# Kernel tuning notes

Measured on AMD Instinct MI355X. Metric: run time of the kernel, lower is better.

The kernel has to match this reference:

```python
import jax, jax.numpy as jnp
import numpy as np

N, E, T, H, O, L = 8192, 262144, 256, 2048, 1024, 128


def setup_inputs() -> dict:
    key = jax.random.key(0)
    ks = jax.random.split(key, 24)
    inp = {}
    inp["eeg_nodes"] = jax.random.normal(ks[0], (N, T), dtype=jnp.float32)
    inp["eeg_idx"] = jax.random.randint(ks[1], (2, E), 0, N, dtype=jnp.int32)
    # PyG models.GIN layer widths: [T->2048], [2048->2048], [2048->2048], [2048->1024]
    dims = [(T, H), (H, H), (H, H), (H, O)]
    k = 2
    for l, (din, dh) in enumerate(dims):
        inp[f"w1_{l}"] = jax.random.normal(ks[k], (din, dh), jnp.float32) / np.float32(np.sqrt(din)); k += 1
        inp[f"b1_{l}"] = jnp.zeros((dh,), jnp.float32)
        inp[f"w2_{l}"] = jax.random.normal(ks[k], (dh, dh), jnp.float32) / np.float32(np.sqrt(dh)); k += 1
        inp[f"b2_{l}"] = jnp.zeros((dh,), jnp.float32)
    inp["wm"] = jax.random.normal(ks[k], (O, L), jnp.float32) / np.float32(np.sqrt(O)); k += 1
    inp["bm"] = jnp.zeros((L,), jnp.float32)
    inp["wv"] = jax.random.normal(ks[k], (O, L), jnp.float32) / np.float32(np.sqrt(O)); k += 1
    inp["bv"] = jnp.zeros((L,), jnp.float32)
    # reparameterize noise (torch.randn_like) made explicit for determinism
    inp["eps"] = jax.random.normal(ks[k + 1], (N, L), jnp.float32)
    return inp


def _gin_conv(x, src, dst, w1, b1, w2, b2):
    # GINConv, eps=0: mlp((1+0)*x + sum_{j->i} x_j); MLP = Linear-ReLU-Linear (no norm)
    agg = jax.ops.segment_sum(x[src], dst, num_segments=x.shape[0])  # [N, d]
    h = jax.nn.relu((x + agg) @ w1 + b1)
    return h @ w2 + b2


def reference(eeg_nodes, eeg_idx, w1_0, b1_0, w2_0, b2_0, w1_1, b1_1, w2_1, b2_1,
              w1_2, b1_2, w2_2, b2_2, w1_3, b1_3, w2_3, b2_3, wm, bm, wv, bv, eps):
    src, dst = eeg_idx[0], eeg_idx[1]
    layers = [(w1_0, b1_0, w2_0, b2_0), (w1_1, b1_1, w2_1, b2_1),
              (w1_2, b1_2, w2_2, b2_2), (w1_3, b1_3, w2_3, b2_3)]
    x = eeg_nodes
    for i, (w1, b1, w2, b2) in enumerate(layers):
        x = _gin_conv(x, src, dst, w1, b1, w2, b2)
        if i < len(layers) - 1:  # BasicGNN: ReLU between convs, not after last
            x = jax.nn.relu(x)
    mean = x @ wm + bm
    var = x @ wv + bv
    z = mean + var * eps  # reparameterize
    return (z, mean, var)
```

## Files before the change

kernel.cpp:

```cpp
#include <hip/hip_runtime.h>

#define NN 8192
#define EE 262144
#define TT 256
#define HH 2048
#define OO 1024
#define LL 128
#define NW 10

typedef __bf16 bf16_t;
typedef __bf16 bf16x8_t __attribute__((ext_vector_type(8)));
typedef float f32x4_t __attribute__((ext_vector_type(4)));

__device__ __forceinline__ void async16(void* lds, const void* g) {
  __builtin_amdgcn_global_load_lds(
      (const __attribute__((address_space(1))) void*)g,
      (__attribute__((address_space(3))) void*)lds, 16, 0, 0);
}


__global__ __launch_bounds__(256) void count_deg_kernel(const int* __restrict__ dst,
                                                        int* __restrict__ deg) {
  int e = blockIdx.x * 256 + threadIdx.x;
  if (e < EE) atomicAdd(&deg[dst[e]], 1);
}

__global__ __launch_bounds__(1024) void scan_kernel(const int* __restrict__ deg,
                                                    int* __restrict__ rs) {
  __shared__ int s[1024];
  int t = threadIdx.x;
  int pre[8];
  int sum = 0;
#pragma unroll
  for (int j = 0; j < 8; ++j) { pre[j] = sum; sum += deg[t * 8 + j]; }
  s[t] = sum;
  __syncthreads();
  for (int off = 1; off < 1024; off <<= 1) {
    int add = (t >= off) ? s[t - off] : 0;
    __syncthreads();
    s[t] += add;
    __syncthreads();
  }
  int base = (t == 0) ? 0 : s[t - 1];
#pragma unroll
  for (int j = 0; j < 8; ++j) rs[t * 8 + j] = base + pre[j];
  if (t == 1023) rs[8192] = s[1023];
}

__global__ __launch_bounds__(256) void fill_csr_kernel(const int* __restrict__ src,
                                                       const int* __restrict__ dst,
                                                       const int* __restrict__ rs,
                                                       int* __restrict__ cur,
                                                       int* __restrict__ csr) {
  int e = blockIdx.x * 256 + threadIdx.x;
  if (e >= EE) return;
  int d = dst[e];
  int p = atomicAdd(&cur[d], 1);
  csr[rs[d] + p] = src[e];
}

struct WTab {
  const float* src[NW];
  int K[NW];
  int N[NW];
  long long dstOff[NW];
  int tileStart[NW + 1];
  const float* x0;
  bf16_t* castDst;
  int castStart;
};

__global__ __launch_bounds__(256) void prep_all_kernel(WTab tab, bf16_t* __restrict__ WT) {
  int b = blockIdx.x;
  int t = threadIdx.x;
  if (b >= tab.castStart) {
    int i = (b - tab.castStart) * 256 + t;
    f32x4_t a = ((const f32x4_t*)tab.x0)[i * 2];
    f32x4_t bb = ((const f32x4_t*)tab.x0)[i * 2 + 1];
    bf16x8_t o;
#pragma unroll
    for (int j = 0; j < 4; ++j) { o[j] = (bf16_t)a[j]; o[4 + j] = (bf16_t)bb[j]; }
    ((bf16x8_t*)tab.castDst)[i] = o;
    return;
  }
  int wi = 0;
#pragma unroll
  for (int k = 1; k < NW; ++k)
    if (b >= tab.tileStart[k]) wi = k;
  int tt = b - tab.tileStart[wi];
  int K = tab.K[wi], N = tab.N[wi];
  int ntn = N >> 6;
  int n0 = (tt % ntn) * 64, k0 = (tt / ntn) * 64;
  const float* in = tab.src[wi];
  bf16_t* out = WT + tab.dstOff[wi];

  __shared__ float tile[64][65];
  for (int c = t; c < 1024; c += 256) {
    int r = c >> 4, col = (c & 15) * 4;
    f32x4_t v = *(const f32x4_t*)&in[(size_t)(k0 + r) * N + n0 + col];
#pragma unroll
    for (int j = 0; j < 4; ++j) tile[r][col + j] = v[j];
  }
  __syncthreads();
  for (int c = t; c < 512; c += 256) {
    int r = c >> 3, col = (c & 7) * 8;
    bf16x8_t v;
#pragma unroll
    for (int j = 0; j < 8; ++j) v[j] = (bf16_t)tile[col + j][r];
    *(bf16x8_t*)&out[(size_t)(n0 + r) * K + k0 + col] = v;
  }
}

__global__ __launch_bounds__(256) void transpose_cast_kernel(const float* __restrict__ in,
                                                             bf16_t* __restrict__ out,
                                                             int K, int N) {
  __shared__ float tile[64][65];
  int n0 = blockIdx.x * 64, k0 = blockIdx.y * 64;
  int t = threadIdx.x;
  for (int c = t; c < 1024; c += 256) {
    int r = c >> 4, col = (c & 15) * 4;
    f32x4_t v = *(const f32x4_t*)&in[(size_t)(k0 + r) * N + n0 + col];
#pragma unroll
    for (int j = 0; j < 4; ++j) tile[r][col + j] = v[j];
  }
  __syncthreads();
  for (int c = t; c < 512; c += 256) {
    int r = c >> 3, col = (c & 7) * 8;
    bf16x8_t v;
#pragma unroll
    for (int j = 0; j < 8; ++j) v[j] = (bf16_t)tile[col + j][r];
    *(bf16x8_t*)&out[(size_t)(n0 + r) * K + k0 + col] = v;
  }
}

__global__ __launch_bounds__(256) void cast_kernel(const float* __restrict__ in,
                                                   bf16_t* __restrict__ out) {
  int i = blockIdx.x * 256 + threadIdx.x;
  f32x4_t a = ((const f32x4_t*)in)[i * 2];
  f32x4_t b = ((const f32x4_t*)in)[i * 2 + 1];
  bf16x8_t o;
#pragma unroll
  for (int j = 0; j < 4; ++j) { o[j] = (bf16_t)a[j]; o[4 + j] = (bf16_t)b[j]; }
  ((bf16x8_t*)out)[i] = o;
}

__global__ __launch_bounds__(64) void agg0_kernel(const bf16_t* __restrict__ x,
                                                  bf16_t* __restrict__ out,
                                                  const int* __restrict__ rs,
                                                  const int* __restrict__ csr) {
  int t = threadIdx.x;
  int node = blockIdx.x * 2 + (t >> 5);
  int c = t & 31;
  const bf16x8_t* xv = (const bf16x8_t*)x;
  bf16x8_t self = xv[(size_t)node * 32 + c];
  float acc[8];
#pragma unroll
  for (int j = 0; j < 8; ++j) acc[j] = (float)self[j];
  int e0 = rs[node], e1 = rs[node + 1];
  int e = e0;
  for (; e + 4 <= e1; e += 4) {
    int s0 = csr[e], s1 = csr[e + 1], s2 = csr[e + 2], s3 = csr[e + 3];
    bf16x8_t v0 = xv[(size_t)s0 * 32 + c];
    bf16x8_t v1 = xv[(size_t)s1 * 32 + c];
    bf16x8_t v2 = xv[(size_t)s2 * 32 + c];
    bf16x8_t v3 = xv[(size_t)s3 * 32 + c];
#pragma unroll
    for (int j = 0; j < 8; ++j)
      acc[j] += (float)v0[j] + (float)v1[j] + (float)v2[j] + (float)v3[j];
  }
  for (; e < e1; ++e) {
    bf16x8_t v = xv[(size_t)csr[e] * 32 + c];
#pragma unroll
    for (int j = 0; j < 8; ++j) acc[j] += (float)v[j];
  }
  bf16x8_t o;
#pragma unroll
  for (int j = 0; j < 8; ++j) o[j] = (bf16_t)acc[j];
  ((bf16x8_t*)out)[(size_t)node * 32 + c] = o;
}

__global__ __launch_bounds__(256) void agg_tiled_kernel(const bf16_t* __restrict__ x,
                                                        bf16_t* __restrict__ out,
                                                        const int* __restrict__ rs,
                                                        const int* __restrict__ csr,
                                                        const float* __restrict__ bias,
                                                        int relu, int tmask, int tshift) {
  int t = threadIdx.x;
  int tile = blockIdx.x & tmask;
  int ng = blockIdx.x >> tshift;
  int node = ng * 8 + (t >> 5);
  int c = t & 31;
  size_t tb = (size_t)tile * (NN * 32);
  const bf16x8_t* xv = (const bf16x8_t*)x + tb;
  bf16x8_t self = xv[node * 32 + c];
  float acc[8];
#pragma unroll
  for (int j = 0; j < 8; ++j) acc[j] = (float)self[j];
  int e0 = rs[node], e1 = rs[node + 1];
  int e = e0;
  for (; e + 4 <= e1; e += 4) {
    int s0 = csr[e], s1 = csr[e + 1], s2 = csr[e + 2], s3 = csr[e + 3];
    bf16x8_t v0 = xv[s0 * 32 + c];
    bf16x8_t v1 = xv[s1 * 32 + c];
    bf16x8_t v2 = xv[s2 * 32 + c];
    bf16x8_t v3 = xv[s3 * 32 + c];
#pragma unroll
    for (int j = 0; j < 8; ++j)
      acc[j] += (float)v0[j] + (float)v1[j] + (float)v2[j] + (float)v3[j];
  }
  for (; e < e1; ++e) {
    bf16x8_t v = xv[csr[e] * 32 + c];
#pragma unroll
    for (int j = 0; j < 8; ++j) acc[j] += (float)v[j];
  }
  if (bias) {
    const float* bp = bias + tile * 256 + c * 8;
    f32x4_t b0 = *(const f32x4_t*)bp;
    f32x4_t b1 = *(const f32x4_t*)(bp + 4);
#pragma unroll
    for (int j = 0; j < 4; ++j) { acc[j] += b0[j]; acc[4 + j] += b1[j]; }
  }
  if (relu) {
#pragma unroll
    for (int j = 0; j < 8; ++j) acc[j] = fmaxf(acc[j], 0.f);
  }
  bf16x8_t o;
#pragma unroll
  for (int j = 0; j < 8; ++j) o[j] = (bf16_t)acc[j];
  ((bf16x8_t*)out + tb)[node * 32 + c] = o;
}

template <int CMODE>
__global__ __launch_bounds__(256, 2) void gemm_bt_kernel(
    const bf16_t* __restrict__ A, const bf16_t* __restrict__ Bt,
    const float* __restrict__ bias, const float* __restrict__ biasB,
    void* __restrict__ Cv, int N, int K, int relu, int nbxShift) {
  __shared__ __align__(16) bf16_t lA[128 * 32];
  __shared__ __align__(16) bf16_t lB[128 * 32];
  const int tid = threadIdx.x;
  const int lane = tid & 63;
  const int wave = tid >> 6;
  const int wm64 = (wave & 1) * 64;
  const int wn64 = (wave >> 1) * 64;
  const int row16 = lane & 15;
  const int quad = lane >> 4;

  const int bid = blockIdx.x;
  const int xcd = bid & 7;
  const int rank = bid >> 3;
  const int bn = rank & ((1 << nbxShift) - 1);
  const int mPer = gridDim.x >> (3 + nbxShift);
  const int bm = xcd * mPer + (rank >> nbxShift);
  const size_t m0 = (size_t)bm * 128;
  const size_t n0 = (size_t)bn * 128;

  f32x4_t acc[4][4];
#pragma unroll
  for (int i = 0; i < 4; ++i)
#pragma unroll
    for (int j = 0; j < 4; ++j)
#pragma unroll
      for (int r = 0; r < 4; ++r) acc[i][j][r] = 0.f;

  const bf16_t* Bbase = Bt + n0 * K;
  const int r0 = tid >> 2;
  const int r1 = (tid + 256) >> 2;
  const int kc = (tid & 3) * 8;

  for (int kt = 0; kt < K; kt += 32) {
    const bf16_t* Ab = A + ((size_t)(kt >> 8)) * (NN * 256) + (kt & 255) + kc;
    async16(&lA[tid * 8], Ab + (m0 + r0) * 256);
    async16(&lA[(tid + 256) * 8], Ab + (m0 + r1) * 256);
    async16(&lB[tid * 8], Bbase + (size_t)r0 * K + kt + kc);
    async16(&lB[(tid + 256) * 8], Bbase + (size_t)r1 * K + kt + kc);
    __syncthreads();
    bf16x8_t af[4], bfr[4];
#pragma unroll
    for (int i = 0; i < 4; ++i)
      af[i] = *(const bf16x8_t*)&lA[(wm64 + i * 16 + row16) * 32 + quad * 8];
#pragma unroll
    for (int i = 0; i < 4; ++i)
      bfr[i] = *(const bf16x8_t*)&lB[(wn64 + i * 16 + row16) * 32 + quad * 8];
#pragma unroll
    for (int i = 0; i < 4; ++i)
#pragma unroll
      for (int j = 0; j < 4; ++j)
        acc[i][j] = __builtin_amdgcn_mfma_f32_16x16x32_bf16(af[i], bfr[j], acc[i][j], 0, 0, 0);
    __syncthreads();
  }

#pragma unroll
  for (int i = 0; i < 4; ++i) {
    size_t row = m0 + wm64 + i * 16 + quad * 4;
#pragma unroll
    for (int j = 0; j < 4; ++j) {
      int col = (int)n0 + wn64 + j * 16 + row16;
      if (CMODE == 0) {
        float b = bias ? bias[col] : 0.f;
        size_t cb = ((size_t)(col >> 8)) * (NN * 256) + (col & 255);
#pragma unroll
        for (int r = 0; r < 4; ++r) {
          float o = acc[i][j][r] + b;
          if (relu) o = fmaxf(o, 0.f);
          ((bf16_t*)Cv)[cb + (row + r) * 256] = (bf16_t)o;
        }
      } else {
        int sel = col >> 7;
        int c2 = col & 127;
        float b = sel ? biasB[c2] : bias[c2];
        float* dstp = (float*)Cv + (size_t)(1 + sel) * NN * LL + c2;
#pragma unroll
        for (int r = 0; r < 4; ++r) {
          dstp[(row + r) * LL] = acc[i][j][r] + b;
        }
      }
    }
  }
}

__global__ __launch_bounds__(512, 1) void gemm256_kernel(
    const bf16_t* __restrict__ A, const bf16_t* __restrict__ Bt,
    const float* __restrict__ bias, bf16_t* __restrict__ C,
    int N, int K, int relu, int nbxShift) {
  __shared__ __align__(16) bf16_t lA[2][256 * 64];
  __shared__ __align__(16) bf16_t lB[2][256 * 64];

  const int t = threadIdx.x;
  const int lane = t & 63;
  const int wave = t >> 6;
  const int wm = wave >> 2;
  const int wn = wave & 3;
  const int row16 = lane & 15;
  const int quad = lane >> 4;
  const int sx = (row16 & 7) << 3;

  const int r0 = t >> 3;
  const int cs = ((t & 7) * 8) ^ ((r0 & 7) << 3);

  const int bid = blockIdx.x;
  const int xcd = bid & 7;
  const int rank = bid >> 3;
  const int bn = rank & ((1 << nbxShift) - 1);
  const int mPer = gridDim.x >> (3 + nbxShift);
  const int bm = xcd * mPer + (rank >> nbxShift);
  const size_t m0 = (size_t)bm * 256;
  const size_t n0 = (size_t)bn * 256;
  const int NT = K >> 6;

  f32x4_t acc[4][4][2];
#pragma unroll
  for (int Q = 0; Q < 4; ++Q)
#pragma unroll
    for (int i = 0; i < 4; ++i)
#pragma unroll
      for (int j = 0; j < 2; ++j)
#pragma unroll
        for (int r = 0; r < 4; ++r) acc[Q][i][j][r] = 0.f;

  bf16x8_t af[4][2], bf[4][2];

#define LOAD_A256(mh)                                                              \
  _Pragma("unroll") for (int i = 0; i < 4; ++i)                                    \
  _Pragma("unroll") for (int ks = 0; ks < 2; ++ks) {                               \
    int row_ = (mh)*128 + wm * 64 + i * 16 + row16;                                \
    af[i][ks] = *(const bf16x8_t*)&lA[c][row_ * 64 + ((ks * 32 + quad * 8) ^ sx)]; \
  }

#define LOAD_B256H(nh)                                                             \
  _Pragma("unroll") for (int j = 0; j < 2; ++j)                                    \
  _Pragma("unroll") for (int ks = 0; ks < 2; ++ks) {                               \
    int row_ = (nh)*128 + wn * 32 + j * 16 + row16;                                \
    bf[(nh)*2 + j][ks] =                                                           \
        *(const bf16x8_t*)&lB[c][row_ * 64 + ((ks * 32 + quad * 8) ^ sx)];         \
  }

#define STAGE_A256(U, mh)                                                            \
  {                                                                                  \
    int u_ = (U);                                                                    \
    int us_ = u_ < NT ? u_ : NT - 1;                                                 \
    int kt_ = us_ << 6;                                                              \
    const bf16_t* g_ = A + (size_t)(kt_ >> 8) * (NN * 256) + (m0 + (mh)*128) * 256 + \
                       (kt_ & 255) + cs;                                             \
    bf16_t* l_ = &lA[u_ & 1][(mh)*8192];                                             \
    async16(l_ + (size_t)t * 8, g_ + (size_t)r0 * 256);                              \
    async16(l_ + (size_t)(t + 512) * 8, g_ + (size_t)(r0 + 64) * 256);               \
  }

#define STAGE_B256(U, nh)                                                  \
  {                                                                        \
    int u_ = (U);                                                          \
    int us_ = u_ < NT ? u_ : NT - 1;                                       \
    int kt_ = us_ << 6;                                                    \
    const bf16_t* g_ = Bt + (n0 + (nh)*128) * (size_t)K + kt_ + cs;        \
    bf16_t* l_ = &lB[u_ & 1][(nh)*8192];                                   \
    async16(l_ + (size_t)t * 8, g_ + (size_t)r0 * K);                      \
    async16(l_ + (size_t)(t + 512) * 8, g_ + (size_t)(r0 + 64) * K);       \
  }

#define MFMA_Q(Q)                                                                    \
  __builtin_amdgcn_s_setprio(1);                                                     \
  _Pragma("unroll") for (int i = 0; i < 4; ++i)                                      \
  _Pragma("unroll") for (int j = 0; j < 2; ++j)                                      \
  _Pragma("unroll") for (int ks = 0; ks < 2; ++ks)                                   \
      acc[Q][i][j] = __builtin_amdgcn_mfma_f32_16x16x32_bf16(                        \
          af[i][ks], bf[(Q & 1) * 2 + j][ks], acc[Q][i][j], 0, 0, 0);                \
  __builtin_amdgcn_s_setprio(0);

#define BAR                                                                \
  do {                                                                     \
    __builtin_amdgcn_sched_barrier(0);                                     \
    asm volatile("s_barrier" ::: "memory");                                \
    __builtin_amdgcn_sched_barrier(0);                                     \
  } while (0)

  STAGE_A256(0, 0); STAGE_B256(0, 0); STAGE_A256(0, 1); STAGE_B256(0, 1);
  asm volatile("" ::: "memory");
  STAGE_A256(1, 0); STAGE_B256(1, 0);
  asm volatile("s_waitcnt vmcnt(4)" ::: "memory");
  BAR;

  for (int T = 0; T < NT; ++T) {
    const int c = T & 1;
    LOAD_A256(0);
    LOAD_B256H(0);
    STAGE_A256(T + 1, 1);
    MFMA_Q(0);
    __builtin_amdgcn_sched_barrier(0);
    LOAD_B256H(1);
    BAR;
    STAGE_B256(T + 1, 1);
    MFMA_Q(1);
    __builtin_amdgcn_sched_barrier(0);
    LOAD_A256(1);
    BAR;
    STAGE_A256(T + 2, 0);
    MFMA_Q(2);
    STAGE_B256(T + 2, 0);
    MFMA_Q(3);
    __builtin_amdgcn_sched_barrier(0);
    asm volatile("s_waitcnt vmcnt(4)" ::: "memory");
    BAR;
  }
  asm volatile("s_waitcnt vmcnt(0)" ::: "memory");

#pragma unroll
  for (int Q = 0; Q < 4; ++Q) {
    const int mh = Q >> 1, nh = Q & 1;
#pragma unroll
    for (int i = 0; i < 4; ++i) {
      size_t row = m0 + mh * 128 + wm * 64 + i * 16 + quad * 4;
#pragma unroll
      for (int j = 0; j < 2; ++j) {
        int col = (int)n0 + nh * 128 + wn * 32 + j * 16 + row16;
        float b = bias ? bias[col] : 0.f;
        size_t cb = ((size_t)(col >> 8)) * (NN * 256) + (col & 255);
#pragma unroll
        for (int r = 0; r < 4; ++r) {
          float o = acc[Q][i][j][r] + b;
          if (relu) o = fmaxf(o, 0.f);
          C[cb + (row + r) * 256] = (bf16_t)o;
        }
      }
    }
  }
#undef LOAD_A256
#undef LOAD_B256H
#undef STAGE_A256
#undef STAGE_B256
#undef MFMA_Q
#undef BAR
}

__global__ __launch_bounds__(256) void reparam_kernel(const float* __restrict__ mean,
                                                      const float* __restrict__ var,
                                                      const float* __restrict__ eps,
                                                      float* __restrict__ z) {
  int i = blockIdx.x * 256 + threadIdx.x;
  f32x4_t m = ((const f32x4_t*)mean)[i];
  f32x4_t v = ((const f32x4_t*)var)[i];
  f32x4_t e = ((const f32x4_t*)eps)[i];
  f32x4_t o;
#pragma unroll
  for (int j = 0; j < 4; ++j) o[j] = m[j] + v[j] * e[j];
  ((f32x4_t*)z)[i] = o;
}

extern "C" void kernel_launch(void* const* d_in, const int* in_sizes, int n_in,
                              void* d_out, int out_size, void* d_ws, size_t ws_size,
                              hipStream_t stream) {
  (void)in_sizes; (void)n_in; (void)out_size;
  const float* x0 = (const float*)d_in[0];
  const int* ei = (const int*)d_in[1];
  const int* src = ei;
  const int* dst = ei + EE;
  const float* w1[4] = {(const float*)d_in[2], (const float*)d_in[6],
                        (const float*)d_in[10], (const float*)d_in[14]};
  const float* b1[4] = {(const float*)d_in[3], (const float*)d_in[7],
                        (const float*)d_in[11], (const float*)d_in[15]};
  const float* w2[4] = {(const float*)d_in[4], (const float*)d_in[8],
                        (const float*)d_in[12], (const float*)d_in[16]};
  const float* b2[4] = {(const float*)d_in[5], (const float*)d_in[9],
                        (const float*)d_in[13], (const float*)d_in[17]};
  const float* wm = (const float*)d_in[18];
  const float* bm = (const float*)d_in[19];
  const float* wv = (const float*)d_in[20];
  const float* bv = (const float*)d_in[21];
  const float* eps = (const float*)d_in[22];
  float* out = (float*)d_out;

  char* ws = (char*)d_ws;
  bf16_t* B0 = (bf16_t*)(ws);
  bf16_t* B1 = (bf16_t*)(ws + 33554432);
  bf16_t* WT = (bf16_t*)(ws + 67108864);

  const long long soff[NW] = {0LL, 524288LL, 4718592LL, 8912896LL, 13107200LL,
                              17301504LL, 21495808LL, 23592960LL, 24641536LL, 24772608LL};
  const size_t wtBytesFull = 24903680ULL * 2ULL;
  const size_t needFull = 67108864ULL + wtBytesFull + 2097152ULL;
  bool full = ws_size >= needFull;

  size_t csrBase = full ? (67108864ULL + wtBytesFull) : 75497472ULL;
  int* deg = (int*)(ws + csrBase);
  int* cur = deg + 8192;
  int* rs = deg + 16384;
  int* csr = deg + 16384 + 8200;

  auto AGG = [&](const bf16_t* in, bf16_t* outp, int d, const float* bias, int relu) {
    int ntiles = d >> 8;
    int tshift = (ntiles == 8) ? 3 : 2;
    agg_tiled_kernel<<<(NN / 8) * ntiles, 256, 0, stream>>>(in, outp, rs, csr, bias, relu,
                                                            ntiles - 1, tshift);
  };

  if (full) {
    WTab tab;
    const float* srcs[NW] = {w1[0], w2[0], w1[1], w2[1], w1[2], w2[2], w1[3], w2[3], wm, wv};
    const int Ks[NW] = {TT, HH, HH, HH, HH, HH, HH, OO, OO, OO};
    const int Ns[NW] = {HH, HH, HH, HH, HH, HH, OO, OO, LL, LL};
    int cum = 0;
    for (int i = 0; i < NW; ++i) {
      tab.src[i] = srcs[i];
      tab.K[i] = Ks[i];
      tab.N[i] = Ns[i];
      tab.dstOff[i] = soff[i];
      tab.tileStart[i] = cum;
      cum += (Ns[i] >> 6) * (Ks[i] >> 6);
    }
    tab.tileStart[NW] = cum;
    tab.castStart = cum;
    tab.x0 = x0;
    tab.castDst = B0;
    int totalBlocks = cum + (NN * TT / 8) / 256;
    prep_all_kernel<<<totalBlocks, 256, 0, stream>>>(tab, WT);

    hipMemsetAsync(deg, 0, 2 * 8192 * sizeof(int), stream);
    count_deg_kernel<<<EE / 256, 256, 0, stream>>>(dst, deg);
    scan_kernel<<<1, 1024, 0, stream>>>(deg, rs);
    fill_csr_kernel<<<EE / 256, 256, 0, stream>>>(src, dst, rs, cur, csr);

    auto G2 = [&](const bf16_t* Ain, int wi, const float* bias, bf16_t* Cout, int K, int relu) {
      gemm256_kernel<<<8 * (NN / 256), 512, 0, stream>>>(Ain, WT + soff[wi], bias, Cout,
                                                         HH, K, relu, 3);
    };
    auto G = [&](const bf16_t* Ain, int wi, const float* bias, bf16_t* Cout, int Nn, int K,
                 int relu) {
      int nbx = Nn / 128;
      int shift = __builtin_ctz(nbx);
      gemm_bt_kernel<0><<<nbx * (NN / 128), 256, 0, stream>>>(
          Ain, WT + soff[wi], bias, nullptr, (void*)Cout, Nn, K, relu, shift);
    };

    agg0_kernel<<<NN / 2, 64, 0, stream>>>(B0, B1, rs, csr);
    G2(B1, 0, b1[0], B0, TT, 1);
    G2(B0, 1, b2[0], B1, HH, 1);
    AGG(B1, B0, HH, nullptr, 0);
    G2(B0, 2, b1[1], B1, HH, 1);
    G2(B1, 3, b2[1], B0, HH, 1);
    AGG(B0, B1, HH, nullptr, 0);
    G2(B1, 4, b1[2], B0, HH, 1);
    G2(B0, 5, b2[2], B1, HH, 1);
    G(B1, 6, nullptr, B0, OO, HH, 0);
    AGG(B0, B1, OO, b1[3], 1);
    G(B1, 7, b2[3], B0, OO, OO, 0);
    gemm_bt_kernel<1><<<2 * (NN / 128), 256, 0, stream>>>(
        B0, WT + soff[8], bm, bv, (void*)out, 256, OO, 0, 1);
  } else {
    hipMemsetAsync(deg, 0, 2 * 8192 * sizeof(int), stream);
    count_deg_kernel<<<EE / 256, 256, 0, stream>>>(dst, deg);
    scan_kernel<<<1, 1024, 0, stream>>>(deg, rs);
    fill_csr_kernel<<<EE / 256, 256, 0, stream>>>(src, dst, rs, cur, csr);

    auto T = [&](const float* w, int K, int Nn, bf16_t* dstw) {
      transpose_cast_kernel<<<dim3(Nn / 64, K / 64), 256, 0, stream>>>(w, dstw, K, Nn);
    };
    auto G2 = [&](const bf16_t* Ain, const float* bias, bf16_t* Cout, int K, int relu) {
      gemm256_kernel<<<8 * (NN / 256), 512, 0, stream>>>(Ain, WT, bias, Cout, HH, K, relu, 3);
    };
    auto G = [&](const bf16_t* Ain, const float* bias, bf16_t* Cout, int Nn, int K, int relu) {
      int nbx = Nn / 128;
      int shift = __builtin_ctz(nbx);
      gemm_bt_kernel<0><<<nbx * (NN / 128), 256, 0, stream>>>(
          Ain, WT, bias, nullptr, (void*)Cout, Nn, K, relu, shift);
    };

    cast_kernel<<<(NN * TT / 8) / 256, 256, 0, stream>>>(x0, B0);
    agg0_kernel<<<NN / 2, 64, 0, stream>>>(B0, B1, rs, csr);
    T(w1[0], TT, HH, WT); G2(B1, b1[0], B0, TT, 1);
    T(w2[0], HH, HH, WT); G2(B0, b2[0], B1, HH, 1);
    AGG(B1, B0, HH, nullptr, 0);
    T(w1[1], HH, HH, WT); G2(B0, b1[1], B1, HH, 1);
    T(w2[1], HH, HH, WT); G2(B1, b2[1], B0, HH, 1);
    AGG(B0, B1, HH, nullptr, 0);
    T(w1[2], HH, HH, WT); G2(B1, b1[2], B0, HH, 1);
    T(w2[2], HH, HH, WT); G2(B0, b2[2], B1, HH, 1);
    T(w1[3], HH, OO, WT); G(B1, nullptr, B0, OO, HH, 0);
    AGG(B0, B1, OO, b1[3], 1);
    T(w2[3], OO, OO, WT); G(B1, b2[3], B0, OO, OO, 0);
    T(wm, OO, LL, WT);
    T(wv, OO, LL, WT + (size_t)LL * OO);
    gemm_bt_kernel<1><<<2 * (NN / 128), 256, 0, stream>>>(
        B0, WT, bm, bv, (void*)out, 256, OO, 0, 1);
  }

  reparam_kernel<<<(NN * LL / 4) / 256, 256, 0, stream>>>(
      out + (size_t)NN * LL, out + (size_t)2 * NN * LL, eps, out);
}
```

Before: 809.9 us.

## Software-pipeline LDS fragment loads across MFMA quadrants in gemm256 kernel

Restructures the main loop of the 256x256 bf16 GEMM so the A/B register fragments for the next quadrant, and for the next K-tile, are read from LDS while the current quadrant's MFMAs run. It uses separate fragment buffers (af1/af2, bfA/bfB) and explicit lgkmcnt/vmcnt waits in place of blanket barriers. The aim is to hide LDS read latency behind matrix-core work. It also raises the launch-bounds minimum to 2 blocks per CU. The doubled LDS buffers (128 KB per block) likely prevent a second block from being co-resident anyway. The tighter register cap risks spilling the 128-float accumulator plus the extra fragment registers.

```diff
diff --git a/kernel.cpp b/kernel.cpp
--- a/kernel.cpp
+++ b/kernel.cpp
@@ -318,7 +318,7 @@
   }
 }
 
-__global__ __launch_bounds__(512, 1) void gemm256_kernel(
+__global__ __launch_bounds__(512, 2) void gemm256_kernel(
     const bf16_t* __restrict__ A, const bf16_t* __restrict__ Bt,
     const float* __restrict__ bias, bf16_t* __restrict__ C,
     int N, int K, int relu, int nbxShift) {
@@ -357,21 +357,20 @@
 #pragma unroll
         for (int r = 0; r < 4; ++r) acc[Q][i][j][r] = 0.f;
 
-  bf16x8_t af[4][2], bf[4][2];
-
-#define LOAD_A256(mh)                                                              \
-  _Pragma("unroll") for (int i = 0; i < 4; ++i)                                    \
-  _Pragma("unroll") for (int ks = 0; ks < 2; ++ks) {                               \
-    int row_ = (mh)*128 + wm * 64 + i * 16 + row16;                                \
-    af[i][ks] = *(const bf16x8_t*)&lA[c][row_ * 64 + ((ks * 32 + quad * 8) ^ sx)]; \
-  }
-
-#define LOAD_B256H(nh)                                                             \
-  _Pragma("unroll") for (int j = 0; j < 2; ++j)                                    \
-  _Pragma("unroll") for (int ks = 0; ks < 2; ++ks) {                               \
-    int row_ = (nh)*128 + wn * 32 + j * 16 + row16;                                \
-    bf[(nh)*2 + j][ks] =                                                           \
-        *(const bf16x8_t*)&lB[c][row_ * 64 + ((ks * 32 + quad * 8) ^ sx)];         \
+  bf16x8_t af1[4][2], af2[4][2], bfA[2][2], bfB[2][2];
+
+#define LOAD_A(dstv, cc, mh)                                                         \
+  _Pragma("unroll") for (int i = 0; i < 4; ++i)                                      \
+  _Pragma("unroll") for (int ks = 0; ks < 2; ++ks) {                                 \
+    int row_ = (mh)*128 + wm * 64 + i * 16 + row16;                                  \
+    dstv[i][ks] = *(const bf16x8_t*)&lA[cc][row_ * 64 + ((ks * 32 + quad * 8) ^ sx)];\
+  }
+
+#define LOAD_B(dstv, cc, nh)                                                         \
+  _Pragma("unroll") for (int j = 0; j < 2; ++j)                                      \
+  _Pragma("unroll") for (int ks = 0; ks < 2; ++ks) {                                 \
+    int row_ = (nh)*128 + wn * 32 + j * 16 + row16;                                  \
+    dstv[j][ks] = *(const bf16x8_t*)&lB[cc][row_ * 64 + ((ks * 32 + quad * 8) ^ sx)];\
   }
 
 #define STAGE_A256(U, mh)                                                            \
@@ -397,13 +396,13 @@
     async16(l_ + (size_t)(t + 512) * 8, g_ + (size_t)(r0 + 64) * K);       \
   }
 
-#define MFMA_Q(Q)                                                                    \
+#define MFMA_Q(Q, AFX, BFX)                                                          \
   __builtin_amdgcn_s_setprio(1);                                                     \
   _Pragma("unroll") for (int i = 0; i < 4; ++i)                                      \
   _Pragma("unroll") for (int j = 0; j < 2; ++j)                                      \
   _Pragma("unroll") for (int ks = 0; ks < 2; ++ks)                                   \
       acc[Q][i][j] = __builtin_amdgcn_mfma_f32_16x16x32_bf16(                        \
-          af[i][ks], bf[(Q & 1) * 2 + j][ks], acc[Q][i][j], 0, 0, 0);                \
+          AFX[i][ks], BFX[j][ks], acc[Q][i][j], 0, 0, 0);                            \
   __builtin_amdgcn_s_setprio(0);
 
 #define BAR                                                                \
@@ -413,33 +412,53 @@
     __builtin_amdgcn_sched_barrier(0);                                     \
   } while (0)
 
-  STAGE_A256(0, 0); STAGE_B256(0, 0); STAGE_A256(0, 1); STAGE_B256(0, 1);
+#define LGKM(n_)                                                           \
+  do {                                                                     \
+    asm volatile("s_waitcnt lgkmcnt(" #n_ ")" ::: "memory");               \
+    __builtin_amdgcn_sched_barrier(0);                                     \
+  } while (0)
+
+#define VMC(n_)                                                            \
+  do {                                                                     \
+    asm volatile("s_waitcnt vmcnt(" #n_ ")" ::: "memory");                 \
+    __builtin_amdgcn_sched_barrier(0);                                     \
+  } while (0)
+
+  STAGE_A256(0, 0); STAGE_B256(0, 0);
+  asm volatile("" ::: "memory");
+  STAGE_A256(0, 1); STAGE_B256(0, 1);
   asm volatile("" ::: "memory");
   STAGE_A256(1, 0); STAGE_B256(1, 0);
-  asm volatile("s_waitcnt vmcnt(4)" ::: "memory");
+  VMC(8);
   BAR;
+  LOAD_A(af1, 0, 0);
+  LOAD_B(bfA, 0, 0);
 
   for (int T = 0; T < NT; ++T) {
     const int c = T & 1;
-    LOAD_A256(0);
-    LOAD_B256H(0);
+    const int n = c ^ 1;
     STAGE_A256(T + 1, 1);
-    MFMA_Q(0);
-    __builtin_amdgcn_sched_barrier(0);
-    LOAD_B256H(1);
+    VMC(6);
     BAR;
+    LOAD_B(bfB, c, 1);
+    LGKM(4);
+    MFMA_Q(0, af1, bfA);
     STAGE_B256(T + 1, 1);
-    MFMA_Q(1);
-    __builtin_amdgcn_sched_barrier(0);
-    LOAD_A256(1);
     BAR;
+    LOAD_A(af2, c, 1);
+    LGKM(8);
+    MFMA_Q(1, af1, bfB);
     STAGE_A256(T + 2, 0);
-    MFMA_Q(2);
+    BAR;
+    LGKM(0);
+    MFMA_Q(2, af2, bfA);
     STAGE_B256(T + 2, 0);
-    MFMA_Q(3);
-    __builtin_amdgcn_sched_barrier(0);
-    asm volatile("s_waitcnt vmcnt(4)" ::: "memory");
+    VMC(8);
     BAR;
+    LOAD_A(af1, n, 0);
+    LOAD_B(bfA, n, 0);
+    LGKM(12);
+    MFMA_Q(3, af2, bfB);
   }
   asm volatile("s_waitcnt vmcnt(0)" ::: "memory");
 
@@ -463,12 +482,14 @@
       }
     }
   }
-#undef LOAD_A256
-#undef LOAD_B256H
+#undef LOAD_A
+#undef LOAD_B
 #undef STAGE_A256
 #undef STAGE_B256
 #undef MFMA_Q
 #undef BAR
+#undef LGKM
+#undef VMC
 }
 
 __global__ __launch_bounds__(256) void reparam_kernel(const float* __restrict__ mean,
```

Measured after the change: 835.7 us. 1.03x slower.

## Pre-pack weights in MFMA fragment order and load B directly to registers

Applied to the files above, without the earlier changes.

Weight transposition now writes the 2048-wide layer weights in a packed layout matching the MFMA fragment order. The 256x256 GEMM then loads B fragments straight from global memory into registers, double-buffered across even and odd tiles, instead of staging them through LDS. Dropping the B LDS buffer halves shared memory use and the launch bound is raised to two blocks per CU. The main loop is rescheduled into two-phase tiles with new waitcnt points. The risk is higher global load latency on the B path and extra register pressure at two waves per SIMD.

```diff
diff --git a/kernel.cpp b/kernel.cpp
--- a/kernel.cpp
+++ b/kernel.cpp
@@ -18,6 +18,14 @@
       (__attribute__((address_space(3))) void*)lds, 16, 0, 0);
 }
 
+
+__device__ __forceinline__ size_t packed_off(int ng, int kg0, int K) {
+  size_t blk = (size_t)(ng >> 8) * (K >> 6) + (kg0 >> 6);
+  int g = ((((ng >> 7) & 1) * 4 + ((ng >> 5) & 3)) * 2 + ((ng >> 4) & 1)) * 2 +
+          ((kg0 & 63) >> 5);
+  int lane_ = (((kg0 >> 3) & 3) << 4) + (ng & 15);
+  return blk * 16384 + (size_t)g * 512 + (size_t)lane_ * 8;
+}
 
 __global__ __launch_bounds__(256) void count_deg_kernel(const int* __restrict__ dst,
                                                         int* __restrict__ deg) {
@@ -63,6 +71,7 @@
   const float* src[NW];
   int K[NW];
   int N[NW];
+  int packed[NW];
   long long dstOff[NW];
   int tileStart[NW + 1];
   const float* x0;
@@ -93,6 +102,7 @@
   int n0 = (tt % ntn) * 64, k0 = (tt / ntn) * 64;
   const float* in = tab.src[wi];
   bf16_t* out = WT + tab.dstOff[wi];
+  int packed = tab.packed[wi];
 
   __shared__ float tile[64][65];
   for (int c = t; c < 1024; c += 256) {
@@ -107,13 +117,17 @@
     bf16x8_t v;
 #pragma unroll
     for (int j = 0; j < 8; ++j) v[j] = (bf16_t)tile[col + j][r];
-    *(bf16x8_t*)&out[(size_t)(n0 + r) * K + k0 + col] = v;
+    if (packed) {
+      *(bf16x8_t*)&out[packed_off(n0 + r, k0 + col, K)] = v;
+    } else {
+      *(bf16x8_t*)&out[(size_t)(n0 + r) * K + k0 + col] = v;
+    }
   }
 }
 
 __global__ __launch_bounds__(256) void transpose_cast_kernel(const float* __restrict__ in,
                                                              bf16_t* __restrict__ out,
-                                                             int K, int N) {
+                                                             int K, int N, int packed) {
   __shared__ float tile[64][65];
   int n0 = blockIdx.x * 64, k0 = blockIdx.y * 64;
   int t = threadIdx.x;
@@ -129,7 +143,11 @@
     bf16x8_t v;
 #pragma unroll
     for (int j = 0; j < 8; ++j) v[j] = (bf16_t)tile[col + j][r];
-    *(bf16x8_t*)&out[(size_t)(n0 + r) * K + k0 + col] = v;
+    if (packed) {
+      *(bf16x8_t*)&out[packed_off(n0 + r, k0 + col, K)] = v;
+    } else {
+      *(bf16x8_t*)&out[(size_t)(n0 + r) * K + k0 + col] = v;
+    }
   }
 }
 
@@ -318,12 +336,11 @@
   }
 }
 
-__global__ __launch_bounds__(512, 1) void gemm256_kernel(
+__global__ __launch_bounds__(512, 2) void gemm256_kernel(
     const bf16_t* __restrict__ A, const bf16_t* __restrict__ Bt,
     const float* __restrict__ bias, bf16_t* __restrict__ C,
     int N, int K, int relu, int nbxShift) {
   __shared__ __align__(16) bf16_t lA[2][256 * 64];
-  __shared__ __align__(16) bf16_t lB[2][256 * 64];
 
   const int t = threadIdx.x;
   const int lane = t & 63;
@@ -357,21 +374,25 @@
 #pragma unroll
         for (int r = 0; r < 4; ++r) acc[Q][i][j][r] = 0.f;
 
-  bf16x8_t af[4][2], bf[4][2];
-
-#define LOAD_A256(mh)                                                              \
-  _Pragma("unroll") for (int i = 0; i < 4; ++i)                                    \
-  _Pragma("unroll") for (int ks = 0; ks < 2; ++ks) {                               \
-    int row_ = (mh)*128 + wm * 64 + i * 16 + row16;                                \
-    af[i][ks] = *(const bf16x8_t*)&lA[c][row_ * 64 + ((ks * 32 + quad * 8) ^ sx)]; \
-  }
-
-#define LOAD_B256H(nh)                                                             \
-  _Pragma("unroll") for (int j = 0; j < 2; ++j)                                    \
-  _Pragma("unroll") for (int ks = 0; ks < 2; ++ks) {                               \
-    int row_ = (nh)*128 + wn * 32 + j * 16 + row16;                                \
-    bf[(nh)*2 + j][ks] =                                                           \
-        *(const bf16x8_t*)&lB[c][row_ * 64 + ((ks * 32 + quad * 8) ^ sx)];         \
+  bf16x8_t af[4][2], bfE[2][2][2], bfO[2][2][2];
+
+#define LOAD_A(cc, mh)                                                              \
+  _Pragma("unroll") for (int i = 0; i < 4; ++i)                                     \
+  _Pragma("unroll") for (int ks = 0; ks < 2; ++ks) {                                \
+    int row_ = (mh)*128 + wm * 64 + i * 16 + row16;                                 \
+    af[i][ks] = *(const bf16x8_t*)&lA[cc][row_ * 64 + ((ks * 32 + quad * 8) ^ sx)]; \
+  }
+
+#define BLOAD(BF, U)                                                                \
+  {                                                                                 \
+    int u_ = (U);                                                                   \
+    int us_ = u_ < NT ? u_ : NT - 1;                                                \
+    const bf16x8_t* bp_ =                                                           \
+        (const bf16x8_t*)(Bt + ((size_t)bn * NT + us_) * 16384) + lane;             \
+    _Pragma("unroll") for (int nh = 0; nh < 2; ++nh)                                \
+    _Pragma("unroll") for (int j = 0; j < 2; ++j)                                   \
+    _Pragma("unroll") for (int ks = 0; ks < 2; ++ks)                                \
+        BF[nh][j][ks] = bp_[((((nh)*4 + wn) * 2 + j) * 2 + ks) * 64];               \
   }
 
 #define STAGE_A256(U, mh)                                                            \
@@ -386,60 +407,54 @@
     async16(l_ + (size_t)(t + 512) * 8, g_ + (size_t)(r0 + 64) * 256);               \
   }
 
-#define STAGE_B256(U, nh)                                                  \
-  {                                                                        \
-    int u_ = (U);                                                          \
-    int us_ = u_ < NT ? u_ : NT - 1;                                       \
-    int kt_ = us_ << 6;                                                    \
-    const bf16_t* g_ = Bt + (n0 + (nh)*128) * (size_t)K + kt_ + cs;        \
-    bf16_t* l_ = &lB[u_ & 1][(nh)*8192];                                   \
-    async16(l_ + (size_t)t * 8, g_ + (size_t)r0 * K);                      \
-    async16(l_ + (size_t)(t + 512) * 8, g_ + (size_t)(r0 + 64) * K);       \
-  }
-
-#define MFMA_Q(Q)                                                                    \
+#define MFMA_PH(mh, BF)                                                              \
   __builtin_amdgcn_s_setprio(1);                                                     \
+  _Pragma("unroll") for (int nh = 0; nh < 2; ++nh)                                   \
   _Pragma("unroll") for (int i = 0; i < 4; ++i)                                      \
   _Pragma("unroll") for (int j = 0; j < 2; ++j)                                      \
   _Pragma("unroll") for (int ks = 0; ks < 2; ++ks)                                   \
-      acc[Q][i][j] = __builtin_amdgcn_mfma_f32_16x16x32_bf16(                        \
-          af[i][ks], bf[(Q & 1) * 2 + j][ks], acc[Q][i][j], 0, 0, 0);                \
+      acc[(mh)*2 + nh][i][j] = __builtin_amdgcn_mfma_f32_16x16x32_bf16(              \
+          af[i][ks], BF[nh][j][ks], acc[(mh)*2 + nh][i][j], 0, 0, 0);                \
   __builtin_amdgcn_s_setprio(0);
 
-#define BAR                                                                \
+#define BARS                                                               \
   do {                                                                     \
     __builtin_amdgcn_sched_barrier(0);                                     \
     asm volatile("s_barrier" ::: "memory");                                \
     __builtin_amdgcn_sched_barrier(0);                                     \
   } while (0)
 
-  STAGE_A256(0, 0); STAGE_B256(0, 0); STAGE_A256(0, 1); STAGE_B256(0, 1);
-  asm volatile("" ::: "memory");
-  STAGE_A256(1, 0); STAGE_B256(1, 0);
-  asm volatile("s_waitcnt vmcnt(4)" ::: "memory");
-  BAR;
-
-  for (int T = 0; T < NT; ++T) {
-    const int c = T & 1;
-    LOAD_A256(0);
-    LOAD_B256H(0);
-    STAGE_A256(T + 1, 1);
-    MFMA_Q(0);
-    __builtin_amdgcn_sched_barrier(0);
-    LOAD_B256H(1);
-    BAR;
-    STAGE_B256(T + 1, 1);
-    MFMA_Q(1);
-    __builtin_amdgcn_sched_barrier(0);
-    LOAD_A256(1);
-    BAR;
-    STAGE_A256(T + 2, 0);
-    MFMA_Q(2);
-    STAGE_B256(T + 2, 0);
-    MFMA_Q(3);
-    __builtin_amdgcn_sched_barrier(0);
-    asm volatile("s_waitcnt vmcnt(4)" ::: "memory");
-    BAR;
+#define VMC(n_)                                                            \
+  do {                                                                     \
+    asm volatile("s_waitcnt vmcnt(" #n_ ")" ::: "memory");                 \
+    __builtin_amdgcn_sched_barrier(0);                                     \
+  } while (0)
+
+#define TILE(X, cc, CUR, NXT)                                              \
+  {                                                                        \
+                                                                  \
+    VMC(2);                                                                \
+    BARS;                                                                  \
+    LOAD_A(cc, 0);                                                         \
+    BLOAD(NXT, (X) + 1);                                                   \
+    STAGE_A256((X) + 1, 0);                                                \
+    MFMA_PH(0, CUR);                                                       \
+                                                                  \
+    VMC(10);                                                               \
+    BARS;                                                                  \
+    LOAD_A(cc, 1);                                                         \
+    STAGE_A256((X) + 1, 1);                                                \
+    MFMA_PH(1, CUR);                                                       \
+  }
+
+  STAGE_A256(0, 0); STAGE_A256(0, 1);
+  BLOAD(bfE, 0);
+  VMC(0);
+  BARS;
+
+  for (int T = 0; T < NT; T += 2) {
+    TILE(T, 0, bfE, bfO);
+    TILE(T + 1, 1, bfO, bfE);
   }
   asm volatile("s_waitcnt vmcnt(0)" ::: "memory");
 
@@ -463,12 +478,13 @@
       }
     }
   }
-#undef LOAD_A256
-#undef LOAD_B256H
+#undef LOAD_A
+#undef BLOAD
 #undef STAGE_A256
-#undef STAGE_B256
-#undef MFMA_Q
-#undef BAR
+#undef MFMA_PH
+#undef BARS
+#undef VMC
+#undef TILE
 }
 
 __global__ __launch_bounds__(256) void reparam_kernel(const float* __restrict__ mean,
@@ -537,11 +553,13 @@
     const float* srcs[NW] = {w1[0], w2[0], w1[1], w2[1], w1[2], w2[2], w1[3], w2[3], wm, wv};
     const int Ks[NW] = {TT, HH, HH, HH, HH, HH, HH, OO, OO, OO};
     const int Ns[NW] = {HH, HH, HH, HH, HH, HH, OO, OO, LL, LL};
+    const int Ps[NW] = {1, 1, 1, 1, 1, 1, 0, 0, 0, 0};
     int cum = 0;
     for (int i = 0; i < NW; ++i) {
       tab.src[i] = srcs[i];
       tab.K[i] = Ks[i];
       tab.N[i] = Ns[i];
+      tab.packed[i] = Ps[i];
       tab.dstOff[i] = soff[i];
       tab.tileStart[i] = cum;
       cum += (Ns[i] >> 6) * (Ks[i] >> 6);
@@ -590,8 +608,8 @@
     scan_kernel<<<1, 1024, 0, stream>>>(deg, rs);
     fill_csr_kernel<<<EE / 256, 256, 0, stream>>>(src, dst, rs, cur, csr);
 
-    auto T = [&](const float* w, int K, int Nn, bf16_t* dstw) {
-      transpose_cast_kernel<<<dim3(Nn / 64, K / 64), 256, 0, stream>>>(w, dstw, K, Nn);
+    auto T = [&](const float* w, int K, int Nn, bf16_t* dstw, int packed) {
+      transpose_cast_kernel<<<dim3(Nn / 64, K / 64), 256, 0, stream>>>(w, dstw, K, Nn, packed);
     };
     auto G2 = [&](const bf16_t* Ain, const float* bias, bf16_t* Cout, int K, int relu) {
       gemm256_kernel<<<8 * (NN / 256), 512, 0, stream>>>(Ain, WT, bias, Cout, HH, K, relu, 3);
@@ -605,19 +623,19 @@
 
     cast_kernel<<<(NN * TT / 8) / 256, 256, 0, stream>>>(x0, B0);
     agg0_kernel<<<NN / 2, 64, 0, stream>>>(B0, B1, rs, csr);
-    T(w1[0], TT, HH, WT); G2(B1, b1[0], B0, TT, 1);
-    T(w2[0], HH, HH, WT); G2(B0, b2[0], B1, HH, 1);
+    T(w1[0], TT, HH, WT, 1); G2(B1, b1[0], B0, TT, 1);
+    T(w2[0], HH, HH, WT, 1); G2(B0, b2[0], B1, HH, 1);
     AGG(B1, B0, HH, nullptr, 0);
-    T(w1[1], HH, HH, WT); G2(B0, b1[1], B1, HH, 1);
-    T(w2[1], HH, HH, WT); G2(B1, b2[1], B0, HH, 1);
+    T(w1[1], HH, HH, WT, 1); G2(B0, b1[1], B1, HH, 1);
+    T(w2[1], HH, HH, WT, 1); G2(B1, b2[1], B0, HH, 1);
     AGG(B0, B1, HH, nullptr, 0);
-    T(w1[2], HH, HH, WT); G2(B1, b1[2], B0, HH, 1);
-    T(w2[2], HH, HH, WT); G2(B0, b2[2], B1, HH, 1);
-    T(w1[3], HH, OO, WT); G(B1, nullptr, B0, OO, HH, 0);
+    T(w1[2], HH, HH, WT, 1); G2(B1, b1[2], B0, HH, 1);
+    T(w2[2], HH, HH, WT, 1); G2(B0, b2[2], B1, HH, 1);
+    T(w1[3], HH, OO, WT, 0); G(B1, nullptr, B0, OO, HH, 0);
     AGG(B0, B1, OO, b1[3], 1);
-    T(w2[3], OO, OO, WT); G(B1, b2[3], B0, OO, OO, 0);
-    T(wm, OO, LL, WT);
-    T(wv, OO, LL, WT + (size_t)LL * OO);
+    T(w2[3], OO, OO, WT, 0); G(B1, b2[3], B0, OO, OO, 0);
+    T(wm, OO, LL, WT, 0);
+    T(wv, OO, LL, WT + (size_t)LL * OO, 0);
     gemm_bt_kernel<1><<<2 * (NN / 128), 256, 0, stream>>>(
         B0, WT, bm, bv, (void*)out, 256, OO, 0, 1);
   }
```

Measured after the change: 828.2 us. +2.3%, slower.
